# Performance work log

Measured on AMD Instinct MI355X. Metric: run time of the kernel, lower is better.

Reference implementation:

```python
import jax, jax.numpy as jnp
import numpy as np

B, N, C, H = 2, 2048, 1024, 16
D = C // H  # head_dim = 64


def setup_inputs() -> dict:
    key = jax.random.key(0)
    ks = jax.random.split(key, 10)
    s = 0.02
    return {
        "x": jax.random.normal(ks[0], (B, N, C), dtype=jnp.float32),
        "gauge_theta": jax.random.normal(ks[1], (C,), dtype=jnp.float32),
        "Wg": jax.random.normal(ks[2], (C, C), dtype=jnp.float32) * s,
        "bg": jnp.zeros((C,), dtype=jnp.float32),
        "Wqkv": jax.random.normal(ks[3], (3 * C, C), dtype=jnp.float32) * s,
        "bqkv": jnp.zeros((3 * C,), dtype=jnp.float32),
        "Wproj": jax.random.normal(ks[4], (C, C), dtype=jnp.float32) * s,
        "bproj": jnp.zeros((C,), dtype=jnp.float32),
    }


def reference(x, gauge_theta, Wg, bg, Wqkv, bqkv, Wproj, bproj):
    # gauge-equivariant mixing: x = x + 0.1 * (Linear(x) * theta)
    x_gauge = (jnp.einsum('bnc,oc->bno', x, Wg) + bg) * gauge_theta  # [B,N,C]
    xg = x + 0.1 * x_gauge
    # fused qkv projection -> [B,N,3,H,D] -> q,k,v [B,H,N,D]
    qkv = (jnp.einsum('bnc,oc->bno', xg, Wqkv) + bqkv).reshape(B, N, 3, H, D)
    qkv = jnp.transpose(qkv, (2, 0, 3, 1, 4))
    q, k, v = qkv[0], qkv[1], qkv[2]
    scale = 1.0 / jnp.sqrt(jnp.float32(D))
    attn = jnp.einsum('bhnd,bhmd->bhnm', q, k) * scale  # explicit [B,H,N,N]
    attn = jax.nn.softmax(attn, axis=-1)  # eval mode: no noise, no dropout
    out = jnp.einsum('bhnm,bhmd->bhnd', attn, v)  # [B,H,N,D]
    out = jnp.transpose(out, (0, 2, 1, 3)).reshape(B, N, C)
    return jnp.einsum('bnc,oc->bno', out, Wproj) + bproj
```

## Files before the change

kernel.cpp:

```cpp
#include <hip/hip_runtime.h>
#include <stdint.h>

typedef __bf16 bf16x8 __attribute__((ext_vector_type(8)));
typedef float  f32x4  __attribute__((ext_vector_type(4)));
typedef unsigned int u32x4 __attribute__((ext_vector_type(4)));
typedef unsigned short u16;

__device__ __forceinline__ u16 f2bf(float f) {
    union { float f; unsigned u; } v; v.f = f;
    unsigned r = v.u + 0x7fffu + ((v.u >> 16) & 1u);
    return (u16)(r >> 16);
}

__device__ __forceinline__ unsigned pk_bf16(float a, float b) {
#if __has_builtin(__builtin_amdgcn_cvt_pk_bf16_f32)
    typedef __bf16 bf16x2_t __attribute__((ext_vector_type(2)));
    bf16x2_t r = __builtin_amdgcn_cvt_pk_bf16_f32(a, b);
    return __builtin_bit_cast(unsigned, r);
#else
    return (unsigned)f2bf(a) | ((unsigned)f2bf(b) << 16);
#endif
}

__device__ __forceinline__ bf16x8 ld_frag(const u16* p) {
    u32x4 u = *(const u32x4*)p;
    return __builtin_bit_cast(bf16x8, u);
}

__device__ __forceinline__ void gload16(const u16* g, u16* l) {
    __builtin_amdgcn_global_load_lds(
        (__attribute__((address_space(1))) void*)g,
        (__attribute__((address_space(3))) void*)l,
        16, 0, 0);
}

#define ATT_CSC 0.18033688011112042f

__global__ __launch_bounds__(256) void cvt_all(
    const float* __restrict__ x, const float* __restrict__ wg,
    const float* __restrict__ wqkv, const float* __restrict__ wproj,
    u16* __restrict__ xo, u16* __restrict__ wgo,
    u16* __restrict__ wqkvo, u16* __restrict__ wprojo)
{
    int i = blockIdx.x * 256 + threadIdx.x;
    const float4* in; uint2* out; int off;
    if (i < 1048576)      { in = (const float4*)x;     out = (uint2*)xo;     off = i; }
    else if (i < 1310720) { in = (const float4*)wg;    out = (uint2*)wgo;    off = i - 1048576; }
    else if (i < 2097152) { in = (const float4*)wqkv;  out = (uint2*)wqkvo;  off = i - 1310720; }
    else                  { in = (const float4*)wproj; out = (uint2*)wprojo; off = i - 2097152; }
    float4 v = in[off];
    uint2 o; o.x = pk_bf16(v.x, v.y); o.y = pk_bf16(v.z, v.w);
    out[off] = o;
}

__global__ __launch_bounds__(256) void gemm_bt(
    const u16* __restrict__ A,
    const u16* __restrict__ W,
    const float* __restrict__ bias,
    u16* __restrict__ qo, u16* __restrict__ ko, u16* __restrict__ vTo)
{
    __shared__ alignas(16) u16 As[128 * 32];
    __shared__ alignas(16) u16 Bs[128 * 32];
    const int tid  = threadIdx.x;
    const int wave = tid >> 6, lane = tid & 63;
    const int lquad = lane >> 4, lcol = lane & 15;
    const int wr = (wave >> 1) * 64, wc = (wave & 1) * 64;
    const int rowb = blockIdx.x * 128, colb = blockIdx.y * 128;
    const int swc = (((lane & 3) ^ ((lane >> 2) & 3)) * 8);
    const int rsw = (lquad ^ (lcol & 3)) * 8;

    const u16* src  = (wave & 2) ? W : A;
    const int  rbase = (wave & 2) ? colb : rowb;
    u16* dst = ((wave & 2) ? Bs : As) + (wave & 1) * 64 * 32;
    const u16* gsrc = src + (size_t)(rbase + (wave & 1) * 64 + (lane >> 2)) * 1024 + swc;

    f32x4 zero4 = {0.f, 0.f, 0.f, 0.f};
    f32x4 acc[4][4];
#pragma unroll
    for (int i = 0; i < 4; i++)
#pragma unroll
        for (int j = 0; j < 4; j++) acc[i][j] = zero4;

    for (int k0 = 0; k0 < 1024; k0 += 32) {
        __syncthreads();
#pragma unroll
        for (int i = 0; i < 4; i++)
            gload16(gsrc + (size_t)(i * 16) * 1024 + k0, dst + i * 16 * 32);
        __syncthreads();
        bf16x8 af[4], bfr[4];
#pragma unroll
        for (int t = 0; t < 4; t++) af[t]  = ld_frag(As + (wr + t * 16 + lcol) * 32 + rsw);
#pragma unroll
        for (int t = 0; t < 4; t++) bfr[t] = ld_frag(Bs + (wc + t * 16 + lcol) * 32 + rsw);
#pragma unroll
        for (int i = 0; i < 4; i++)
#pragma unroll
            for (int j = 0; j < 4; j++)
                acc[i][j] = __builtin_amdgcn_mfma_f32_16x16x32_bf16(af[i], bfr[j], acc[i][j], 0, 0, 0);
    }

#pragma unroll
    for (int i = 0; i < 4; i++) {
#pragma unroll
        for (int j = 0; j < 4; j++) {
            int gcol = colb + wc + j * 16 + lcol;
            float bsv = bias[gcol];
            int grow0 = rowb + wr + i * 16 + lquad * 4;
            int three = gcol >> 10, rem = gcol & 1023;
            int h = rem >> 6, d = rem & 63;
            int b = grow0 >> 11, nn = grow0 & 2047;
            int bh = b * 16 + h;
            if (three == 2) {
                ushort4 o;
                o.x = f2bf(acc[i][j][0] + bsv);
                o.y = f2bf(acc[i][j][1] + bsv);
                o.z = f2bf(acc[i][j][2] + bsv);
                o.w = f2bf(acc[i][j][3] + bsv);
                *(ushort4*)(vTo + ((size_t)bh * 64 + d) * 2048 + nn) = o;
            } else if (three == 0) {
#pragma unroll
                for (int r = 0; r < 4; r++)
                    qo[((size_t)bh * 2048 + nn + r) * 64 + d] = f2bf((acc[i][j][r] + bsv) * ATT_CSC);
            } else {
#pragma unroll
                for (int r = 0; r < 4; r++)
                    ko[((size_t)bh * 2048 + nn + r) * 64 + d] = f2bf(acc[i][j][r] + bsv);
            }
        }
    }
}

__global__ __launch_bounds__(256) void gemm64(
    int mode,
    const u16* __restrict__ A,
    const u16* __restrict__ W,
    const float* __restrict__ bias,
    const float* __restrict__ xres,
    const float* __restrict__ theta,
    u16* __restrict__ out_bf,
    float* __restrict__ out_f)
{
    __shared__ alignas(16) u16 As[64 * 32];
    __shared__ alignas(16) u16 Bs[128 * 32];
    const int tid  = threadIdx.x;
    const int wave = tid >> 6, lane = tid & 63;
    const int lquad = lane >> 4, lcol = lane & 15;
    const int wr = (wave & 1) * 32, wc = (wave >> 1) * 64;
    const int rowb = blockIdx.x * 64, colb = blockIdx.y * 128;
    const int swc = (((lane & 3) ^ ((lane >> 2) & 3)) * 8);
    const int rsw = (lquad ^ (lcol & 3)) * 8;

    const u16* gp[3]; u16* lp[3];
#pragma unroll
    for (int t = 0; t < 3; t++) {
        int id = wave + t * 4;
        if (id < 4) {
            gp[t] = A + (size_t)(rowb + id * 16 + (lane >> 2)) * 1024 + swc;
            lp[t] = As + id * 512;
        } else {
            int g = id - 4;
            gp[t] = W + (size_t)(colb + g * 16 + (lane >> 2)) * 1024 + swc;
            lp[t] = Bs + g * 512;
        }
    }

    f32x4 zero4 = {0.f, 0.f, 0.f, 0.f};
    f32x4 acc[2][4];
#pragma unroll
    for (int i = 0; i < 2; i++)
#pragma unroll
        for (int j = 0; j < 4; j++) acc[i][j] = zero4;

    for (int k0 = 0; k0 < 1024; k0 += 32) {
        __syncthreads();
#pragma unroll
        for (int t = 0; t < 3; t++)
            gload16(gp[t] + k0, lp[t]);
        __syncthreads();
        bf16x8 af[2], bfr[4];
#pragma unroll
        for (int t = 0; t < 2; t++) af[t]  = ld_frag(As + (wr + t * 16 + lcol) * 32 + rsw);
#pragma unroll
        for (int t = 0; t < 4; t++) bfr[t] = ld_frag(Bs + (wc + t * 16 + lcol) * 32 + rsw);
#pragma unroll
        for (int i = 0; i < 2; i++)
#pragma unroll
            for (int j = 0; j < 4; j++)
                acc[i][j] = __builtin_amdgcn_mfma_f32_16x16x32_bf16(af[i], bfr[j], acc[i][j], 0, 0, 0);
    }

#pragma unroll
    for (int i = 0; i < 2; i++) {
#pragma unroll
        for (int j = 0; j < 4; j++) {
            int gcol = colb + wc + j * 16 + lcol;
            float bsv = bias[gcol];
            int grow0 = rowb + wr + i * 16 + lquad * 4;
            if (mode == 0) {
#pragma unroll
                for (int r = 0; r < 4; r++) {
                    size_t idx = (size_t)(grow0 + r) * 1024 + gcol;
                    float val = acc[i][j][r] + bsv;
                    out_bf[idx] = f2bf(xres[idx] + 0.1f * (val * theta[gcol]));
                }
            } else {
#pragma unroll
                for (int r = 0; r < 4; r++)
                    out_f[(size_t)(grow0 + r) * 1024 + gcol] = acc[i][j][r] + bsv;
            }
        }
    }
}

__global__ __launch_bounds__(256) void attn_kernel(
    const u16* __restrict__ q,
    const u16* __restrict__ k,
    const u16* __restrict__ vT,
    u16* __restrict__ attnout)
{
    __shared__ alignas(16) u16 Ks[2][2 * 2 * 64 * 32];
    __shared__ alignas(16) u16 Vs[2][2 * 2 * 64 * 32];

    const int tid  = threadIdx.x;
    const int wave = tid >> 6, lane = tid & 63;
    const int lquad = lane >> 4, lcol = lane & 15;
    const int bh   = blockIdx.y;
    const int row0 = blockIdx.x * 128 + wave * 32;
    const int rsw  = (lquad ^ (lcol & 3)) * 8;

    bf16x8 qf[2][2];
#pragma unroll
    for (int qh = 0; qh < 2; qh++)
#pragma unroll
        for (int db = 0; db < 2; db++)
            qf[qh][db] = ld_frag(q + ((size_t)bh * 2048 + row0 + qh * 16 + lcol) * 64 + db * 32 + lquad * 8);

    const int sb = wave & 1;
    const int srow = lane >> 2;
    const int swc  = (((lane & 3) ^ (srow & 3)) * 8);
    const u16* gK = k  + ((size_t)bh * 2048 + srow) * 64 + sb * 32 + swc;
    const u16* gV = vT + ((size_t)bh * 64 + srow) * 2048 + sb * 32 + swc;

    auto stage = [&](int j0, int buf) {
        u16* ldst = ((wave & 2) ? Vs[buf] : Ks[buf]) + sb * 64 * 32;
        if ((wave & 2) == 0) {
#pragma unroll
            for (int jh = 0; jh < 2; jh++)
#pragma unroll
                for (int i = 0; i < 4; i++)
                    gload16(gK + (size_t)(j0 + jh * 64 + i * 16) * 64, ldst + jh * 4096 + i * 16 * 32);
        } else {
#pragma unroll
            for (int jh = 0; jh < 2; jh++)
#pragma unroll
                for (int i = 0; i < 4; i++)
                    gload16(gV + (size_t)(i * 16) * 2048 + j0 + jh * 64, ldst + jh * 4096 + i * 16 * 32);
        }
    };

    f32x4 zero4 = {0.f, 0.f, 0.f, 0.f};
    f32x4 lacc[2] = {zero4, zero4};
    f32x4 oacc[2][4];
#pragma unroll
    for (int qh = 0; qh < 2; qh++)
#pragma unroll
        for (int dt = 0; dt < 4; dt++) oacc[qh][dt] = zero4;

    stage(0, 0);
    __syncthreads();

    for (int it = 0; it < 16; ++it) {
        const int buf = it & 1;
        if (it < 15) stage((it + 1) * 128, buf ^ 1);

#pragma unroll
        for (int jh = 0; jh < 2; jh++) {
            const u16* Ksb = Ks[buf] + jh * 4096;
            const u16* Vsb = Vs[buf] + jh * 4096;

            f32x4 sacc[2][4];
#pragma unroll
            for (int qh = 0; qh < 2; qh++)
#pragma unroll
                for (int jt = 0; jt < 4; jt++) sacc[qh][jt] = zero4;
            __builtin_amdgcn_s_setprio(1);
#pragma unroll
            for (int jt = 0; jt < 4; jt++)
#pragma unroll
                for (int db = 0; db < 2; db++) {
                    bf16x8 kf = ld_frag(Ksb + db * 64 * 32 + (jt * 16 + lcol) * 32 + rsw);
#pragma unroll
                    for (int qh = 0; qh < 2; qh++)
                        sacc[qh][jt] = __builtin_amdgcn_mfma_f32_16x16x32_bf16(kf, qf[qh][db], sacc[qh][jt], 0, 0, 0);
                }
            __builtin_amdgcn_s_setprio(0);

            unsigned dpk[2][4][2];
#pragma unroll
            for (int qh = 0; qh < 2; qh++) {
#pragma unroll
                for (int jt = 0; jt < 4; jt++) {
                    f32x4 pe;
                    pe[0] = __builtin_amdgcn_exp2f(sacc[qh][jt][0]);
                    pe[1] = __builtin_amdgcn_exp2f(sacc[qh][jt][1]);
                    pe[2] = __builtin_amdgcn_exp2f(sacc[qh][jt][2]);
                    pe[3] = __builtin_amdgcn_exp2f(sacc[qh][jt][3]);
                    lacc[qh] += pe;
                    dpk[qh][jt][0] = pk_bf16(pe[0], pe[1]);
                    dpk[qh][jt][1] = pk_bf16(pe[2], pe[3]);
                }
            }

            bf16x8 pf[2][2];
#pragma unroll
            for (int qh = 0; qh < 2; qh++) {
#pragma unroll
                for (int kb = 0; kb < 2; kb++) {
                    unsigned Ax = dpk[qh][2 * kb][0],     Ay = dpk[qh][2 * kb][1];
                    unsigned Bx = dpk[qh][2 * kb + 1][0], By = dpk[qh][2 * kb + 1][1];
                    u32x4 w;
#if __has_builtin(__builtin_amdgcn_permlane32_swap) && __has_builtin(__builtin_amdgcn_permlane16_swap)
                    {
                        auto s1 = __builtin_amdgcn_permlane32_swap(Ax, Bx, false, false);
                        auto s2 = __builtin_amdgcn_permlane16_swap(s1[0], s1[1], false, false);
                        w[0] = s2[0]; w[2] = s2[1];
                        auto s3 = __builtin_amdgcn_permlane32_swap(Ay, By, false, false);
                        auto s4 = __builtin_amdgcn_permlane16_swap(s3[0], s3[1], false, false);
                        w[1] = s4[0]; w[3] = s4[1];
                    }
#else
                    {
                        unsigned x1x = (lquad < 2) ? Bx : Ax;
                        unsigned x1y = (lquad < 2) ? By : Ay;
                        unsigned r1x = __shfl_xor(x1x, 32, 64);
                        unsigned r1y = __shfl_xor(x1y, 32, 64);
                        unsigned x2x = (lquad == 1) ? Ax : (lquad == 2) ? Bx : r1x;
                        unsigned x2y = (lquad == 1) ? Ay : (lquad == 2) ? By : r1y;
                        unsigned r2x = __shfl_xor(x2x, 16, 64);
                        unsigned r2y = __shfl_xor(x2y, 16, 64);
                        w[0] = (lquad == 0) ? Ax : (lquad == 2) ? r1x : r2x;
                        w[1] = (lquad == 0) ? Ay : (lquad == 2) ? r1y : r2y;
                        w[2] = (lquad == 1) ? r1x : (lquad == 3) ? Bx : r2x;
                        w[3] = (lquad == 1) ? r1y : (lquad == 3) ? By : r2y;
                    }
#endif
                    pf[qh][kb] = __builtin_bit_cast(bf16x8, w);
                }
            }

            __builtin_amdgcn_s_setprio(1);
#pragma unroll
            for (int dt = 0; dt < 4; dt++)
#pragma unroll
                for (int kb = 0; kb < 2; kb++) {
                    bf16x8 vf = ld_frag(Vsb + kb * 64 * 32 + (dt * 16 + lcol) * 32 + rsw);
#pragma unroll
                    for (int qh = 0; qh < 2; qh++)
                        oacc[qh][dt] = __builtin_amdgcn_mfma_f32_16x16x32_bf16(vf, pf[qh][kb], oacc[qh][dt], 0, 0, 0);
                }
            __builtin_amdgcn_s_setprio(0);
        }

        __syncthreads();
    }

    const int b = bh >> 4, h = bh & 15;
#pragma unroll
    for (int qh = 0; qh < 2; qh++) {
        float l = (lacc[qh][0] + lacc[qh][1]) + (lacc[qh][2] + lacc[qh][3]);
        l += __shfl_xor(l, 16, 64);
        l += __shfl_xor(l, 32, 64);
        float inv = 1.0f / l;
        const int n = row0 + qh * 16 + lcol;
        size_t base = ((size_t)b * 2048 + n) * 1024 + h * 64;
#pragma unroll
        for (int dt = 0; dt < 4; dt++) {
            uint2 o;
            o.x = pk_bf16(oacc[qh][dt][0] * inv, oacc[qh][dt][1] * inv);
            o.y = pk_bf16(oacc[qh][dt][2] * inv, oacc[qh][dt][3] * inv);
            *(uint2*)(attnout + base + dt * 16 + lquad * 4) = o;
        }
    }
}

extern "C" void kernel_launch(void* const* d_in, const int* in_sizes, int n_in,
                              void* d_out, int out_size, void* d_ws, size_t ws_size,
                              hipStream_t stream) {
    const float* x     = (const float*)d_in[0];
    const float* theta = (const float*)d_in[1];
    const float* Wg    = (const float*)d_in[2];
    const float* bg    = (const float*)d_in[3];
    const float* Wqkv  = (const float*)d_in[4];
    const float* bqkv  = (const float*)d_in[5];
    const float* Wproj = (const float*)d_in[6];
    const float* bproj = (const float*)d_in[7];
    float* out = (float*)d_out;

    unsigned char* ws = (unsigned char*)d_ws;
    const size_t MB = 1ull << 20;
    u16* x_bf     = (u16*)(ws + 0);
    u16* Wg_bf    = (u16*)(ws + 8 * MB);
    u16* Wqkv_bf  = (u16*)(ws + 10 * MB);
    u16* Wproj_bf = (u16*)(ws + 16 * MB);
    u16* xg_bf    = (u16*)(ws + 18 * MB);
    u16* q_bf     = (u16*)(ws + 26 * MB);
    u16* k_bf     = (u16*)(ws + 34 * MB);
    u16* vT_bf    = (u16*)(ws + 42 * MB);
    u16* ao_bf    = (u16*)(ws + 50 * MB);

    dim3 blk(256);
    cvt_all<<<9216, blk, 0, stream>>>(x, Wg, Wqkv, Wproj,
                                      x_bf, Wg_bf, Wqkv_bf, Wproj_bf);

    gemm64<<<dim3(64, 8), blk, 0, stream>>>(0, x_bf, Wg_bf, bg,
                                            x, theta, xg_bf, nullptr);
    gemm_bt<<<dim3(32, 24), blk, 0, stream>>>(xg_bf, Wqkv_bf, bqkv,
                                              q_bf, k_bf, vT_bf);
    attn_kernel<<<dim3(16, 32), blk, 0, stream>>>(q_bf, k_bf, vT_bf, ao_bf);
    gemm64<<<dim3(64, 8), blk, 0, stream>>>(2, ao_bf, Wproj_bf, bproj,
                                            nullptr, nullptr, nullptr, out);
}
```

Baseline: 236.6 us.

## Split attention key range across two wave groups with shared-memory reduction

Result: faster. 230.9 us (-2.4%).

```diff
diff --git a/kernel.cpp b/kernel.cpp
--- a/kernel.cpp
+++ b/kernel.cpp
@@ -212,21 +212,24 @@
     }
 }
 
-__global__ __launch_bounds__(256) void attn_kernel(
+__global__ __launch_bounds__(512, 4) void attn_kernel(
     const u16* __restrict__ q,
     const u16* __restrict__ k,
     const u16* __restrict__ vT,
     u16* __restrict__ attnout)
 {
-    __shared__ alignas(16) u16 Ks[2][2 * 2 * 64 * 32];
-    __shared__ alignas(16) u16 Vs[2][2 * 2 * 64 * 32];
+    __shared__ alignas(16) u16 smem[32768];
 
     const int tid  = threadIdx.x;
     const int wave = tid >> 6, lane = tid & 63;
+    const int g = wave >> 2, wq = wave & 3;
     const int lquad = lane >> 4, lcol = lane & 15;
     const int bh   = blockIdx.y;
-    const int row0 = blockIdx.x * 128 + wave * 32;
+    const int row0 = blockIdx.x * 128 + wq * 32;
     const int rsw  = (lquad ^ (lcol & 3)) * 8;
+
+    u16* KsG = smem + g * 8192;
+    u16* VsG = smem + 16384 + g * 8192;
 
     bf16x8 qf[2][2];
 #pragma unroll
@@ -235,26 +238,24 @@
         for (int db = 0; db < 2; db++)
             qf[qh][db] = ld_frag(q + ((size_t)bh * 2048 + row0 + qh * 16 + lcol) * 64 + db * 32 + lquad * 8);
 
-    const int sb = wave & 1;
+    const int sb = wq & 1;
     const int srow = lane >> 2;
     const int swc  = (((lane & 3) ^ (srow & 3)) * 8);
     const u16* gK = k  + ((size_t)bh * 2048 + srow) * 64 + sb * 32 + swc;
     const u16* gV = vT + ((size_t)bh * 64 + srow) * 2048 + sb * 32 + swc;
 
-    auto stage = [&](int j0, int buf) {
-        u16* ldst = ((wave & 2) ? Vs[buf] : Ks[buf]) + sb * 64 * 32;
-        if ((wave & 2) == 0) {
-#pragma unroll
-            for (int jh = 0; jh < 2; jh++)
-#pragma unroll
-                for (int i = 0; i < 4; i++)
-                    gload16(gK + (size_t)(j0 + jh * 64 + i * 16) * 64, ldst + jh * 4096 + i * 16 * 32);
+    auto stage = [&](int it, int buf) {
+        int j0 = g * 1024 + it * 64;
+        if ((wq & 2) == 0) {
+            u16* ldst = KsG + buf * 4096 + sb * 2048;
+#pragma unroll
+            for (int i = 0; i < 4; i++)
+                gload16(gK + (size_t)(j0 + i * 16) * 64, ldst + i * 16 * 32);
         } else {
-#pragma unroll
-            for (int jh = 0; jh < 2; jh++)
-#pragma unroll
-                for (int i = 0; i < 4; i++)
-                    gload16(gV + (size_t)(i * 16) * 2048 + j0 + jh * 64, ldst + jh * 4096 + i * 16 * 32);
+            u16* ldst = VsG + buf * 4096 + sb * 2048;
+#pragma unroll
+            for (int i = 0; i < 4; i++)
+                gload16(gV + (size_t)(i * 16) * 2048 + j0, ldst + i * 16 * 32);
         }
     };
 
@@ -271,97 +272,116 @@
 
     for (int it = 0; it < 16; ++it) {
         const int buf = it & 1;
-        if (it < 15) stage((it + 1) * 128, buf ^ 1);
-
-#pragma unroll
-        for (int jh = 0; jh < 2; jh++) {
-            const u16* Ksb = Ks[buf] + jh * 4096;
-            const u16* Vsb = Vs[buf] + jh * 4096;
-
-            f32x4 sacc[2][4];
-#pragma unroll
-            for (int qh = 0; qh < 2; qh++)
-#pragma unroll
-                for (int jt = 0; jt < 4; jt++) sacc[qh][jt] = zero4;
-            __builtin_amdgcn_s_setprio(1);
-#pragma unroll
-            for (int jt = 0; jt < 4; jt++)
-#pragma unroll
-                for (int db = 0; db < 2; db++) {
-                    bf16x8 kf = ld_frag(Ksb + db * 64 * 32 + (jt * 16 + lcol) * 32 + rsw);
-#pragma unroll
-                    for (int qh = 0; qh < 2; qh++)
-                        sacc[qh][jt] = __builtin_amdgcn_mfma_f32_16x16x32_bf16(kf, qf[qh][db], sacc[qh][jt], 0, 0, 0);
+        if (it < 15) stage(it + 1, buf ^ 1);
+
+        const u16* Kt = KsG + buf * 4096;
+        const u16* Vt = VsG + buf * 4096;
+
+        f32x4 sacc[2][4];
+#pragma unroll
+        for (int qh = 0; qh < 2; qh++)
+#pragma unroll
+            for (int jt = 0; jt < 4; jt++) sacc[qh][jt] = zero4;
+        __builtin_amdgcn_s_setprio(1);
+#pragma unroll
+        for (int jt = 0; jt < 4; jt++)
+#pragma unroll
+            for (int db = 0; db < 2; db++) {
+                bf16x8 kf = ld_frag(Kt + db * 2048 + (jt * 16 + lcol) * 32 + rsw);
+#pragma unroll
+                for (int qh = 0; qh < 2; qh++)
+                    sacc[qh][jt] = __builtin_amdgcn_mfma_f32_16x16x32_bf16(kf, qf[qh][db], sacc[qh][jt], 0, 0, 0);
+            }
+        __builtin_amdgcn_s_setprio(0);
+
+        unsigned dpk[2][4][2];
+#pragma unroll
+        for (int qh = 0; qh < 2; qh++) {
+#pragma unroll
+            for (int jt = 0; jt < 4; jt++) {
+                f32x4 pe;
+                pe[0] = __builtin_amdgcn_exp2f(sacc[qh][jt][0]);
+                pe[1] = __builtin_amdgcn_exp2f(sacc[qh][jt][1]);
+                pe[2] = __builtin_amdgcn_exp2f(sacc[qh][jt][2]);
+                pe[3] = __builtin_amdgcn_exp2f(sacc[qh][jt][3]);
+                lacc[qh] += pe;
+                dpk[qh][jt][0] = pk_bf16(pe[0], pe[1]);
+                dpk[qh][jt][1] = pk_bf16(pe[2], pe[3]);
+            }
+        }
+
+        bf16x8 pf[2][2];
+#pragma unroll
+        for (int qh = 0; qh < 2; qh++) {
+#pragma unroll
+            for (int kb = 0; kb < 2; kb++) {
+                unsigned Ax = dpk[qh][2 * kb][0],     Ay = dpk[qh][2 * kb][1];
+                unsigned Bx = dpk[qh][2 * kb + 1][0], By = dpk[qh][2 * kb + 1][1];
+                u32x4 w;
+#if __has_builtin(__builtin_amdgcn_permlane32_swap) && __has_builtin(__builtin_amdgcn_permlane16_swap)
+                {
+                    auto s1 = __builtin_amdgcn_permlane32_swap(Ax, Bx, false, false);
+                    auto s2 = __builtin_amdgcn_permlane16_swap(s1[0], s1[1], false, false);
+                    w[0] = s2[0]; w[2] = s2[1];
+                    auto s3 = __builtin_amdgcn_permlane32_swap(Ay, By, false, false);
+                    auto s4 = __builtin_amdgcn_permlane16_swap(s3[0], s3[1], false, false);
+                    w[1] = s4[0]; w[3] = s4[1];
                 }
-            __builtin_amdgcn_s_setprio(0);
-
-            unsigned dpk[2][4][2];
-#pragma unroll
-            for (int qh = 0; qh < 2; qh++) {
-#pragma unroll
-                for (int jt = 0; jt < 4; jt++) {
-                    f32x4 pe;
-                    pe[0] = __builtin_amdgcn_exp2f(sacc[qh][jt][0]);
-                    pe[1] = __builtin_amdgcn_exp2f(sacc[qh][jt][1]);
-                    pe[2] = __builtin_amdgcn_exp2f(sacc[qh][jt][2]);
-                    pe[3] = __builtin_amdgcn_exp2f(sacc[qh][jt][3]);
-                    lacc[qh] += pe;
-                    dpk[qh][jt][0] = pk_bf16(pe[0], pe[1]);
-                    dpk[qh][jt][1] = pk_bf16(pe[2], pe[3]);
+#else
+                {
+                    unsigned x1x = (lquad < 2) ? Bx : Ax;
+                    unsigned x1y = (lquad < 2) ? By : Ay;
+                    unsigned r1x = __shfl_xor(x1x, 32, 64);
+                    unsigned r1y = __shfl_xor(x1y, 32, 64);
+                    unsigned x2x = (lquad == 1) ? Ax : (lquad == 2) ? Bx : r1x;
+                    unsigned x2y = (lquad == 1) ? Ay : (lquad == 2) ? By : r1y;
+                    unsigned r2x = __shfl_xor(x2x, 16, 64);
+                    unsigned r2y = __shfl_xor(x2y, 16, 64);
+                    w[0] = (lquad == 0) ? Ax : (lquad == 2) ? r1x : r2x;
+                    w[1] = (lquad == 0) ? Ay : (lquad == 2) ? r1y : r2y;
+                    w[2] = (lquad == 1) ? r1x : (lquad == 3) ? Bx : r2x;
+                    w[3] = (lquad == 1) ? r1y : (lquad == 3) ? By : r2y;
                 }
-            }
-
-            bf16x8 pf[2][2];
-#pragma unroll
-            for (int qh = 0; qh < 2; qh++) {
-#pragma unroll
-                for (int kb = 0; kb < 2; kb++) {
-                    unsigned Ax = dpk[qh][2 * kb][0],     Ay = dpk[qh][2 * kb][1];
-                    unsigned Bx = dpk[qh][2 * kb + 1][0], By = dpk[qh][2 * kb + 1][1];
-                    u32x4 w;
-#if __has_builtin(__builtin_amdgcn_permlane32_swap) && __has_builtin(__builtin_amdgcn_permlane16_swap)
-                    {
-                        auto s1 = __builtin_amdgcn_permlane32_swap(Ax, Bx, false, false);
-                        auto s2 = __builtin_amdgcn_permlane16_swap(s1[0], s1[1], false, false);
-                        w[0] = s2[0]; w[2] = s2[1];
-                        auto s3 = __builtin_amdgcn_permlane32_swap(Ay, By, false, false);
-                        auto s4 = __builtin_amdgcn_permlane16_swap(s3[0], s3[1], false, false);
-                        w[1] = s4[0]; w[3] = s4[1];
-                    }
-#else
-                    {
-                        unsigned x1x = (lquad < 2) ? Bx : Ax;
-                        unsigned x1y = (lquad < 2) ? By : Ay;
-                        unsigned r1x = __shfl_xor(x1x, 32, 64);
-                        unsigned r1y = __shfl_xor(x1y, 32, 64);
-                        unsigned x2x = (lquad == 1) ? Ax : (lquad == 2) ? Bx : r1x;
-                        unsigned x2y = (lquad == 1) ? Ay : (lquad == 2) ? By : r1y;
-                        unsigned r2x = __shfl_xor(x2x, 16, 64);
-                        unsigned r2y = __shfl_xor(x2y, 16, 64);
-                        w[0] = (lquad == 0) ? Ax : (lquad == 2) ? r1x : r2x;
-                        w[1] = (lquad == 0) ? Ay : (lquad == 2) ? r1y : r2y;
-                        w[2] = (lquad == 1) ? r1x : (lquad == 3) ? Bx : r2x;
-                        w[3] = (lquad == 1) ? r1y : (lquad == 3) ? By : r2y;
-                    }
 #endif
-                    pf[qh][kb] = __builtin_bit_cast(bf16x8, w);
-                }
-            }
-
-            __builtin_amdgcn_s_setprio(1);
+                pf[qh][kb] = __builtin_bit_cast(bf16x8, w);
+            }
+        }
+
+        __builtin_amdgcn_s_setprio(1);
+#pragma unroll
+        for (int dt = 0; dt < 4; dt++)
+#pragma unroll
+            for (int kb = 0; kb < 2; kb++) {
+                bf16x8 vf = ld_frag(Vt + kb * 2048 + (dt * 16 + lcol) * 32 + rsw);
+#pragma unroll
+                for (int qh = 0; qh < 2; qh++)
+                    oacc[qh][dt] = __builtin_amdgcn_mfma_f32_16x16x32_bf16(vf, pf[qh][kb], oacc[qh][dt], 0, 0, 0);
+            }
+        __builtin_amdgcn_s_setprio(0);
+
+        __syncthreads();
+    }
+
+    float* scr = (float*)smem;
+    const int slot = wq * 64 + lane;
+    if (g == 1) {
+#pragma unroll
+        for (int qh = 0; qh < 2; qh++) {
 #pragma unroll
             for (int dt = 0; dt < 4; dt++)
-#pragma unroll
-                for (int kb = 0; kb < 2; kb++) {
-                    bf16x8 vf = ld_frag(Vsb + kb * 64 * 32 + (dt * 16 + lcol) * 32 + rsw);
-#pragma unroll
-                    for (int qh = 0; qh < 2; qh++)
-                        oacc[qh][dt] = __builtin_amdgcn_mfma_f32_16x16x32_bf16(vf, pf[qh][kb], oacc[qh][dt], 0, 0, 0);
-                }
-            __builtin_amdgcn_s_setprio(0);
-        }
-
-        __syncthreads();
+                *(f32x4*)&scr[slot * 44 + qh * 16 + dt * 4] = oacc[qh][dt];
+            *(f32x4*)&scr[slot * 44 + 32 + qh * 4] = lacc[qh];
+        }
+    }
+    __syncthreads();
+    if (g == 1) return;
+
+#pragma unroll
+    for (int qh = 0; qh < 2; qh++) {
+#pragma unroll
+        for (int dt = 0; dt < 4; dt++)
+            oacc[qh][dt] += *(const f32x4*)&scr[slot * 44 + qh * 16 + dt * 4];
+        lacc[qh] += *(const f32x4*)&scr[slot * 44 + 32 + qh * 4];
     }
 
     const int b = bh >> 4, h = bh & 15;
@@ -416,7 +436,7 @@
                                             x, theta, xg_bf, nullptr);
     gemm_bt<<<dim3(32, 24), blk, 0, stream>>>(xg_bf, Wqkv_bf, bqkv,
                                               q_bf, k_bf, vT_bf);
-    attn_kernel<<<dim3(16, 32), blk, 0, stream>>>(q_bf, k_bf, vT_bf, ao_bf);
+    attn_kernel<<<dim3(16, 32), dim3(512), 0, stream>>>(q_bf, k_bf, vT_bf, ao_bf);
     gemm64<<<dim3(64, 8), blk, 0, stream>>>(2, ao_bf, Wproj_bf, bproj,
                                             nullptr, nullptr, nullptr, out);
 }
```
